# Optimization experiments

Measured on AMD Instinct MI355X. Metric: run time of the kernel, lower is better.

The kernel has to match this reference:

```python
import jax, jax.numpy as jnp
import numpy as np

T_V = 0.1
T_Q = 0.1
NEG_VIDEO_IOU = 0.5
POS_VIDEO_TOPK = 1
MARGIN = 0.0
EPS = 1e-12


def _normalize(x):
    # F.normalize(dim=-1) with eps clamp
    n = jnp.linalg.norm(x, axis=-1, keepdims=True)
    return x / jnp.maximum(n, EPS)


def _log_cross_entropy(pos_score, all_score, neg_mask, t, m):
    pos_exp = jnp.exp((pos_score - m) / t)
    neg_exp_sum = jnp.sum(jnp.exp(all_score / t) * neg_mask, axis=-1)
    loss = -((pos_score - m) / t - jnp.log(pos_exp + neg_exp_sum))
    return jnp.mean(loss)


def setup_inputs() -> dict:
    B, C, N, S = 32, 256, 64, 64
    key = jax.random.key(0)
    k1, k2, k3 = jax.random.split(key, 3)
    video_feats = jax.random.normal(k1, (B, C, N, N), dtype=jnp.float32)
    sents_feats = jax.random.normal(k2, (S, C), dtype=jnp.float32)
    iou2ds = jax.random.uniform(k3, (S, N, N), dtype=jnp.float32)
    mask2d = jnp.triu(jnp.ones((N, N), dtype=bool))  # P = N*(N+1)/2 = 2080
    num_targets = jnp.full((B,), S // B, dtype=jnp.int32)  # sums to S
    return {"video_feats": video_feats, "sents_feats": sents_feats,
            "num_targets": num_targets, "iou2ds": iou2ds, "mask2d": mask2d}


def reference(video_feats, sents_feats, num_targets, iou2ds, mask2d):
    B, C, N, _ = video_feats.shape
    S = sents_feats.shape[0]
    K = POS_VIDEO_TOPK
    # mask2d / num_targets are structural constants -> resolve on host
    flat_idx = np.nonzero(np.asarray(mask2d).reshape(-1))[0]   # [P]
    P = flat_idx.shape[0]
    scatter_idx = np.repeat(np.arange(B), np.asarray(num_targets))  # [S]

    # masked_select of valid proposals
    vf = video_feats.reshape(B, C, N * N)[:, :, flat_idx]      # [B,C,P]
    vf = jnp.transpose(vf, (0, 2, 1))                          # [B,P,C]
    iou = iou2ds.reshape(S, N * N)[:, flat_idx]                # [S,P]

    vf = _normalize(vf)
    sf = _normalize(sents_feats)                               # [S,C]

    # top-k proposals per sentence
    topk_idx = jax.lax.top_k(iou, K)[1]                        # [S,K]
    sv = vf[scatter_idx]                                       # [S,P,C]
    topk_video = jnp.take_along_axis(sv, topk_idx[:, :, None], axis=1)  # [S,K,C]

    # inter-video loss
    inter_video_pos = jnp.einsum('skc,sc->sk', topk_video, sf)          # [S,K]
    inter_video_all = jnp.einsum('skc,tc->skt', topk_video, sf)         # [S,K,S]
    inter_video_neg_mask = (~jnp.eye(S, dtype=bool))[:, None, :]        # [S,1,S]
    loss_inter_video = _log_cross_entropy(
        inter_video_pos, inter_video_all, inter_video_neg_mask, T_V, MARGIN)

    # inter-query loss
    inter_query_all = jnp.einsum('sc,bpc->sbp', sf, vf).reshape(S, 1, B * P)
    same_video = jnp.asarray(scatter_idx)[:, None] == jnp.arange(B)[None, :]  # [S,B]
    pos_mask = same_video[:, :, None] & (iou > NEG_VIDEO_IOU)[:, None, :]     # [S,B,P]
    inter_query_neg_mask = (~pos_mask).reshape(S, 1, B * P)
    loss_inter_query = _log_cross_entropy(
        inter_video_pos, inter_query_all, inter_query_neg_mask, T_Q, MARGIN)

    return (loss_inter_video, loss_inter_query)
```

## Files before the change

### kernel.cpp

```cpp
#include <hip/hip_runtime.h>
#include <hip/hip_bf16.h>
#include <math.h>

constexpr int B_ = 32;
constexpr int C_ = 256;
constexpr int N_ = 64;
constexpr int S_ = 64;
constexpr int NPIX = N_ * N_;
constexpr int QB = B_ * N_;
constexpr int RG = 32;

#define T_V_INV 10.0f
#define T_Q_INV 10.0f
#define NEG_IOU 0.5f

typedef __attribute__((ext_vector_type(8))) short short8;
typedef __attribute__((ext_vector_type(4))) float f32x4;

static __device__ __forceinline__ unsigned short f2bf(float x) {
  __hip_bfloat16 h = __float2bfloat16(x);
  unsigned short u;
  __builtin_memcpy(&u, &h, sizeof(u));
  return u;
}

__global__ __launch_bounds__(256) void k_setup(
    const float* __restrict__ sents, const float* __restrict__ iou,
    const int* __restrict__ nt,
    float* __restrict__ sf_t, unsigned short* __restrict__ sf_frag,
    int* __restrict__ scatter, int* __restrict__ top_pix) {
  int bid = blockIdx.x, tid = threadIdx.x;
  __shared__ float wsum[4];
  __shared__ float bval[256];
  __shared__ int bidx[256];

  if (bid < S_) {
    int s = bid, c = tid;
    float v = sents[s * C_ + c];
    float ss = v * v;
    #pragma unroll
    for (int o = 32; o; o >>= 1) ss += __shfl_xor(ss, o);
    if ((c & 63) == 0) wsum[c >> 6] = ss;
    __syncthreads();
    float tot = wsum[0] + wsum[1] + wsum[2] + wsum[3];
    float rn = 1.0f / fmaxf(sqrtf(tot), 1e-12f);
    float o = v * rn;
    sf_t[c * S_ + s] = o;
    int ks = c >> 5, q = (c >> 3) & 3, j = c & 7;
    int mt = s >> 4, m = s & 15;
    sf_frag[((ks * 4 + mt) * 64 + (q * 16 + m)) * 8 + j] = f2bf(o);

    float bv = -1.0f;
    int bi = 0x7fffffff;
    for (int pix = tid; pix < NPIX; pix += 256) {
      int r = pix >> 6, c0 = pix & 63;
      if (c0 >= r) {
        float x = iou[s * NPIX + pix];
        if (x > bv) { bv = x; bi = pix; }
      }
    }
    bval[tid] = bv; bidx[tid] = bi;
    __syncthreads();
    for (int st = 128; st; st >>= 1) {
      if (tid < st) {
        float ov = bval[tid + st]; int oi = bidx[tid + st];
        if (ov > bval[tid] || (ov == bval[tid] && oi < bidx[tid])) {
          bval[tid] = ov; bidx[tid] = oi;
        }
      }
      __syncthreads();
    }
    if (tid == 0) top_pix[s] = bidx[0];
  } else {
    if (tid < S_) {
      int cum = 0, res = 0;
      for (int b = 0; b < B_; b++) {
        int nb = nt[b];
        if (tid >= cum && tid < cum + nb) res = b;
        cum += nb;
      }
      scatter[tid] = res;
    }
  }
}

__global__ __launch_bounds__(256) void k_main(
    const float* __restrict__ V, const float* __restrict__ iou,
    const short8* __restrict__ Afrag, const float* __restrict__ sf_t,
    const int* __restrict__ scatter, const int* __restrict__ top_pix,
    float* __restrict__ partials, float* __restrict__ pos_score,
    float* __restrict__ loss_vid) {
  __shared__ int ssc[S_];
  __shared__ float part[4][S_];
  __shared__ float vh[C_];
  __shared__ float red[4];
  __shared__ float pdm[4][S_];

  int tid = threadIdx.x;

  if (blockIdx.x < QB) {
    if (tid < S_) ssc[tid] = scatter[tid];
    __syncthreads();

    int b = blockIdx.x >> 6, r = blockIdx.x & 63;
    int w = tid >> 6, lane = tid & 63;
    int n = lane & 15, q = lane >> 4;
    int col = w * 16 + n;
    int pix = r * 64 + col;
    bool active = (col >= r);

    const float* vb = V + (size_t)b * C_ * NPIX + pix;
    f32x4 acc[4] = {f32x4{0,0,0,0}, f32x4{0,0,0,0}, f32x4{0,0,0,0}, f32x4{0,0,0,0}};
    float ssq = 0.0f;

    for (int ks = 0; ks < 8; ks++) {
      short8 bfrag;
      #pragma unroll
      for (int j = 0; j < 8; j++) {
        int c = ks * 32 + q * 8 + j;
        float v = active ? vb[(size_t)c * NPIX] : 0.0f;
        ssq = fmaf(v, v, ssq);
        bfrag[j] = (short)f2bf(v);
      }
      #pragma unroll
      for (int mt = 0; mt < 4; mt++) {
        short8 a = Afrag[(ks * 4 + mt) * 64 + lane];
        acc[mt] = __builtin_amdgcn_mfma_f32_16x16x32_bf16(a, bfrag, acc[mt], 0, 0, 0);
      }
    }

    ssq += __shfl_xor(ssq, 16);
    ssq += __shfl_xor(ssq, 32);
    float rs = T_Q_INV / fmaxf(sqrtf(ssq), 1e-12f);

    #pragma unroll
    for (int mt = 0; mt < 4; mt++) {
      #pragma unroll
      for (int rr = 0; rr < 4; rr++) {
        int s = mt * 16 + q * 4 + rr;
        float e = active ? __expf(acc[mt][rr] * rs) : 0.0f;
        if (active && ssc[s] == b) {
          if (iou[s * NPIX + pix] > NEG_IOU) e = 0.0f;
        }
        e += __shfl_xor(e, 1);
        e += __shfl_xor(e, 2);
        e += __shfl_xor(e, 4);
        e += __shfl_xor(e, 8);
        if (n == 0) part[w][s] = e;
      }
    }
    __syncthreads();
    if (tid < S_) {
      partials[(size_t)blockIdx.x * S_ + tid] =
          part[0][tid] + part[1][tid] + part[2][tid] + part[3][tid];
    }
  } else {
    int s = blockIdx.x - QB;
    int b = scatter[s];
    int pix = top_pix[s];
    float v = V[((size_t)b * C_ + tid) * NPIX + pix];
    float ss = v * v;
    #pragma unroll
    for (int o = 32; o; o >>= 1) ss += __shfl_xor(ss, o);
    if ((tid & 63) == 0) red[tid >> 6] = ss;
    __syncthreads();
    float tot = red[0] + red[1] + red[2] + red[3];
    float rn = 1.0f / fmaxf(sqrtf(tot), 1e-12f);
    vh[tid] = v * rn;
    __syncthreads();
    int so = tid & 63, chunk = tid >> 6;
    float pd = 0.0f;
    #pragma unroll 8
    for (int c = chunk * 64; c < chunk * 64 + 64; c++)
      pd = fmaf(vh[c], sf_t[c * S_ + so], pd);
    pdm[chunk][so] = pd;
    __syncthreads();
    if (tid < S_) {
      float dot = pdm[0][tid] + pdm[1][tid] + pdm[2][tid] + pdm[3][tid];
      if (tid == s) pos_score[s] = dot;
      float pos = __shfl(dot, s);
      float e = (tid == s) ? 0.0f : __expf(dot * T_V_INV);
      #pragma unroll
      for (int o = 32; o; o >>= 1) e += __shfl_xor(e, o);
      if (tid == 0) {
        float pp = pos * T_V_INV;
        loss_vid[s] = -(pp - logf(__expf(pp) + e));
      }
    }
  }
}

__global__ __launch_bounds__(256) void k_red(
    const float* __restrict__ partials, float* __restrict__ neg1) {
  int g = blockIdx.x, tid = threadIdx.x;
  int j = tid >> 6, s = tid & 63;
  __shared__ float m[4][S_];
  float acc = 0.0f;
  #pragma unroll
  for (int k = 0; k < 16; k++)
    acc += partials[(size_t)((g * 64 + j * 16 + k)) * S_ + s];
  m[j][s] = acc;
  __syncthreads();
  if (tid < S_)
    neg1[g * S_ + tid] = m[0][tid] + m[1][tid] + m[2][tid] + m[3][tid];
}

__global__ __launch_bounds__(256) void k_fin(
    const float* __restrict__ neg1, const float* __restrict__ pos_score,
    const float* __restrict__ loss_vid, float* __restrict__ out) {
  int tid = threadIdx.x;
  int j = tid >> 6, s = tid & 63;
  __shared__ float m[4][S_];
  float acc = 0.0f;
  #pragma unroll
  for (int i = 0; i < 8; i++) acc += neg1[(j * 8 + i) * S_ + s];
  m[j][s] = acc;
  __syncthreads();
  if (tid < S_) {
    float neg = m[0][tid] + m[1][tid] + m[2][tid] + m[3][tid];
    float p = pos_score[tid] * T_Q_INV;
    float lq = -(p - logf(__expf(p) + neg));
    float lv = loss_vid[tid];
    #pragma unroll
    for (int o = 32; o; o >>= 1) {
      lq += __shfl_xor(lq, o);
      lv += __shfl_xor(lv, o);
    }
    if (tid == 0) {
      out[0] = lv / (float)S_;
      out[1] = lq / (float)S_;
    }
  }
}

extern "C" void kernel_launch(void* const* d_in, const int* in_sizes, int n_in,
                              void* d_out, int out_size, void* d_ws, size_t ws_size,
                              hipStream_t stream) {
  const float* V     = (const float*)d_in[0];
  const float* sents = (const float*)d_in[1];
  const int*   nt    = (const int*)d_in[2];
  const float* iou   = (const float*)d_in[3];

  float* ws = (float*)d_ws;
  float*          sf_t    = ws;
  unsigned short* sf_frag = (unsigned short*)(ws + 16384);
  int*   scatter   = (int*)(ws + 16384 + 8192);
  int*   top_pix   = scatter + S_;
  float* pos_score = (float*)(top_pix + S_);
  float* loss_vid  = pos_score + S_;
  float* partials  = loss_vid + S_;
  float* neg1      = partials + (size_t)QB * S_;

  k_setup<<<S_ + 1, 256, 0, stream>>>(sents, iou, nt, sf_t, sf_frag, scatter, top_pix);
  k_main <<<QB + S_, 256, 0, stream>>>(V, iou, (const short8*)sf_frag, sf_t,
                                       scatter, top_pix, partials, pos_score, loss_vid);
  k_red  <<<RG, 256, 0, stream>>>(partials, neg1);
  k_fin  <<<1, 256, 0, stream>>>(neg1, pos_score, loss_vid, (float*)d_out);
}
```

Before: 221.8 us.

## Compact triangular proposals into dense tiles, stage A fragments in LDS, merge reductions

The main kernel now walks a compacted list of the 2080 upper-triangular pixels, built once in setup as a lookup table. This removes roughly half of the wasted lanes and blocks that the per-row layout spent on masked-out pixels. All 64 channel values per lane are loaded up front into registers, and the sentence fragments are staged in shared memory so loads can overlap. The separate two-stage partial reduction is replaced by one 1024-thread final kernel, which saves a launch. The costs are higher register pressure from the 64-float array, gathered rather than contiguous pixel addresses, and a larger LDS footprint that may limit occupancy.

Measured after the change: 213.4 us (median of 2 runs). 3.8% less time.

```diff
diff --git a/kernel.cpp b/kernel.cpp
--- a/kernel.cpp
+++ b/kernel.cpp
@@ -7,8 +7,9 @@
 constexpr int N_ = 64;
 constexpr int S_ = 64;
 constexpr int NPIX = N_ * N_;
-constexpr int QB = B_ * N_;
-constexpr int RG = 32;
+constexpr int P_ = 2080;
+constexpr int TPB = 33;
+constexpr int NQ = TPB * B_;
 
 #define T_V_INV 10.0f
 #define T_Q_INV 10.0f
@@ -28,7 +29,8 @@
     const float* __restrict__ sents, const float* __restrict__ iou,
     const int* __restrict__ nt,
     float* __restrict__ sf_t, unsigned short* __restrict__ sf_frag,
-    int* __restrict__ scatter, int* __restrict__ top_pix) {
+    int* __restrict__ scatter, int* __restrict__ top_pix,
+    int* __restrict__ tab) {
   int bid = blockIdx.x, tid = threadIdx.x;
   __shared__ float wsum[4];
   __shared__ float bval[256];
@@ -81,6 +83,13 @@
       }
       scatter[tid] = res;
     }
+    for (int pix = tid; pix < NPIX; pix += 256) {
+      int r = pix >> 6, c0 = pix & 63;
+      if (c0 >= r) {
+        int t = r * 64 - (r * (r - 1)) / 2 + (c0 - r);
+        tab[t] = pix;
+      }
+    }
   }
 }
 
@@ -88,43 +97,58 @@
     const float* __restrict__ V, const float* __restrict__ iou,
     const short8* __restrict__ Afrag, const float* __restrict__ sf_t,
     const int* __restrict__ scatter, const int* __restrict__ top_pix,
+    const int* __restrict__ tab,
     float* __restrict__ partials, float* __restrict__ pos_score,
     float* __restrict__ loss_vid) {
   __shared__ int ssc[S_];
   __shared__ float part[4][S_];
+  __shared__ short8 afr[32 * 64];
   __shared__ float vh[C_];
   __shared__ float red[4];
   __shared__ float pdm[4][S_];
 
   int tid = threadIdx.x;
 
-  if (blockIdx.x < QB) {
+  if (blockIdx.x < NQ) {
     if (tid < S_) ssc[tid] = scatter[tid];
-    __syncthreads();
-
-    int b = blockIdx.x >> 6, r = blockIdx.x & 63;
+    for (int i = tid; i < 32 * 64; i += 256) afr[i] = Afrag[i];
+    __syncthreads();
+
+    int v = blockIdx.x / TPB, blk = blockIdx.x % TPB;
     int w = tid >> 6, lane = tid & 63;
     int n = lane & 15, q = lane >> 4;
-    int col = w * 16 + n;
-    int pix = r * 64 + col;
-    bool active = (col >= r);
-
-    const float* vb = V + (size_t)b * C_ * NPIX + pix;
+    int t = blk * 64 + w * 16 + n;
+    bool valid = (t < P_);
+    int tt = valid ? t : (P_ - 1);
+    int pix = tab[tt];
+
+    const float* vb = V + (size_t)v * C_ * NPIX + pix;
+    const float* vbq = vb + (size_t)(q * 8) * NPIX;
+
+    float vv[64];
+    #pragma unroll
+    for (int ks = 0; ks < 8; ks++) {
+      #pragma unroll
+      for (int j = 0; j < 8; j++) {
+        vv[ks * 8 + j] = vbq[(size_t)(ks * 32 + j) * NPIX];
+      }
+    }
+
     f32x4 acc[4] = {f32x4{0,0,0,0}, f32x4{0,0,0,0}, f32x4{0,0,0,0}, f32x4{0,0,0,0}};
     float ssq = 0.0f;
 
+    #pragma unroll
     for (int ks = 0; ks < 8; ks++) {
       short8 bfrag;
       #pragma unroll
       for (int j = 0; j < 8; j++) {
-        int c = ks * 32 + q * 8 + j;
-        float v = active ? vb[(size_t)c * NPIX] : 0.0f;
-        ssq = fmaf(v, v, ssq);
-        bfrag[j] = (short)f2bf(v);
+        float x = vv[ks * 8 + j];
+        ssq = fmaf(x, x, ssq);
+        bfrag[j] = (short)f2bf(x);
       }
       #pragma unroll
       for (int mt = 0; mt < 4; mt++) {
-        short8 a = Afrag[(ks * 4 + mt) * 64 + lane];
+        short8 a = afr[(ks * 4 + mt) * 64 + lane];
         acc[mt] = __builtin_amdgcn_mfma_f32_16x16x32_bf16(a, bfrag, acc[mt], 0, 0, 0);
       }
     }
@@ -138,8 +162,8 @@
       #pragma unroll
       for (int rr = 0; rr < 4; rr++) {
         int s = mt * 16 + q * 4 + rr;
-        float e = active ? __expf(acc[mt][rr] * rs) : 0.0f;
-        if (active && ssc[s] == b) {
+        float e = valid ? __expf(acc[mt][rr] * rs) : 0.0f;
+        if (valid && ssc[s] == v) {
           if (iou[s * NPIX + pix] > NEG_IOU) e = 0.0f;
         }
         e += __shfl_xor(e, 1);
@@ -155,7 +179,7 @@
           part[0][tid] + part[1][tid] + part[2][tid] + part[3][tid];
     }
   } else {
-    int s = blockIdx.x - QB;
+    int s = blockIdx.x - NQ;
     int b = scatter[s];
     int pix = top_pix[s];
     float v = V[((size_t)b * C_ + tid) * NPIX + pix];
@@ -190,34 +214,23 @@
   }
 }
 
-__global__ __launch_bounds__(256) void k_red(
-    const float* __restrict__ partials, float* __restrict__ neg1) {
-  int g = blockIdx.x, tid = threadIdx.x;
-  int j = tid >> 6, s = tid & 63;
-  __shared__ float m[4][S_];
-  float acc = 0.0f;
-  #pragma unroll
-  for (int k = 0; k < 16; k++)
-    acc += partials[(size_t)((g * 64 + j * 16 + k)) * S_ + s];
-  m[j][s] = acc;
-  __syncthreads();
-  if (tid < S_)
-    neg1[g * S_ + tid] = m[0][tid] + m[1][tid] + m[2][tid] + m[3][tid];
-}
-
-__global__ __launch_bounds__(256) void k_fin(
-    const float* __restrict__ neg1, const float* __restrict__ pos_score,
+__global__ __launch_bounds__(1024) void k_fin(
+    const float* __restrict__ partials, const float* __restrict__ pos_score,
     const float* __restrict__ loss_vid, float* __restrict__ out) {
   int tid = threadIdx.x;
-  int j = tid >> 6, s = tid & 63;
-  __shared__ float m[4][S_];
-  float acc = 0.0f;
-  #pragma unroll
-  for (int i = 0; i < 8; i++) acc += neg1[(j * 8 + i) * S_ + s];
-  m[j][s] = acc;
+  __shared__ f32x4 m[64][16];
+  const f32x4* p4 = (const f32x4*)partials;
+  int s4 = tid & 15, g = tid >> 4;
+  f32x4 a = {0.0f, 0.0f, 0.0f, 0.0f};
+  #pragma unroll 4
+  for (int i = g; i < NQ; i += 64) a += p4[i * 16 + s4];
+  m[g][s4] = a;
   __syncthreads();
   if (tid < S_) {
-    float neg = m[0][tid] + m[1][tid] + m[2][tid] + m[3][tid];
+    int q4 = tid >> 2, e4 = tid & 3;
+    float neg = 0.0f;
+    #pragma unroll
+    for (int g2 = 0; g2 < 64; g2++) neg += m[g2][q4][e4];
     float p = pos_score[tid] * T_Q_INV;
     float lq = -(p - logf(__expf(p) + neg));
     float lv = loss_vid[tid];
@@ -248,12 +261,13 @@
   int*   top_pix   = scatter + S_;
   float* pos_score = (float*)(top_pix + S_);
   float* loss_vid  = pos_score + S_;
-  float* partials  = loss_vid + S_;
-  float* neg1      = partials + (size_t)QB * S_;
-
-  k_setup<<<S_ + 1, 256, 0, stream>>>(sents, iou, nt, sf_t, sf_frag, scatter, top_pix);
-  k_main <<<QB + S_, 256, 0, stream>>>(V, iou, (const short8*)sf_frag, sf_t,
-                                       scatter, top_pix, partials, pos_score, loss_vid);
-  k_red  <<<RG, 256, 0, stream>>>(partials, neg1);
-  k_fin  <<<1, 256, 0, stream>>>(neg1, pos_score, loss_vid, (float*)d_out);
-}
+  int*   tab       = (int*)(loss_vid + S_);
+  float* partials  = (float*)(tab + TPB * 64);
+
+  k_setup<<<S_ + 1, 256, 0, stream>>>(sents, iou, nt, sf_t, sf_frag, scatter,
+                                      top_pix, tab);
+  k_main <<<NQ + S_, 256, 0, stream>>>(V, iou, (const short8*)sf_frag, sf_t,
+                                       scatter, top_pix, tab, partials,
+                                       pos_score, loss_vid);
+  k_fin  <<<1, 1024, 0, stream>>>(partials, pos_score, loss_vid, (float*)d_out);
+}
```
